# Kernel optimization log

Measured on AMD Instinct MI355X. Metric: run time of the kernel, lower is better.

Reference implementation:

```python
import jax, jax.numpy as jnp
import numpy as np

N_GAUSS = 2048
FEAT_DIM = 3
IMG_H, IMG_W = 256, 256
EPS = 1e-4  # args.eps with tiled rasterizer path


def setup_inputs() -> dict:
    key = jax.random.key(0)
    k_xy, k_sc, k_rot, k_feat = jax.random.split(key, 4)
    xy = jax.random.uniform(k_xy, (N_GAUSS, 2), dtype=jnp.float32)  # normalized [0,1) coords
    # scale holds INVERSE std-devs (disable_inverse_scale=False path: scale = 1/init_scale);
    # values 10..50 give Gaussians spanning a few pixels at 256x256.
    scale = jax.random.uniform(k_sc, (N_GAUSS, 2), minval=10.0, maxval=50.0, dtype=jnp.float32)
    rot = jax.random.normal(k_rot, (N_GAUSS, 1), dtype=jnp.float32)
    feat = jax.random.uniform(k_feat, (N_GAUSS, FEAT_DIM), dtype=jnp.float32)
    return {"xy": xy, "scale": scale, "rot": rot, "feat": feat, "topk": 8}


def reference(xy, scale, rot, feat, topk):
    # Pixel centers in normalized coordinates, matching get_grid(h, w) -> (x, y)
    xs = (jnp.arange(IMG_W, dtype=jnp.float32) + 0.5) / IMG_W
    ys = (jnp.arange(IMG_H, dtype=jnp.float32) + 0.5) / IMG_H
    px, py = jnp.meshgrid(xs, ys, indexing="xy")  # each [H, W]
    px = px.reshape(-1)  # [P]
    py = py.reshape(-1)

    dx = px[:, None] - xy[None, :, 0]  # [P, N]
    dy = py[:, None] - xy[None, :, 1]  # [P, N]

    c = jnp.cos(rot[:, 0])  # [N]
    s = jnp.sin(rot[:, 0])
    # Rotate offset into the Gaussian's local frame
    lx = dx * c + dy * s   # [P, N]
    ly = -dx * s + dy * c  # [P, N]

    # Anisotropic Gaussian weight; scale is the inverse std-dev per axis
    w = jnp.exp(-0.5 * ((lx * scale[:, 0]) ** 2 + (ly * scale[:, 1]) ** 2))  # [P, N]

    # Keep top-k Gaussians per pixel, normalize their weights, accumulate features
    tw, ti = jax.lax.top_k(w, topk)        # [P, K]
    tf = feat[ti]                          # [P, K, C]
    alpha = tw / (jnp.sum(tw, axis=-1, keepdims=True) + EPS)  # [P, K]
    img = jnp.einsum("pk,pkc->pc", alpha, tf)                 # [P, C]
    return img.reshape(IMG_H, IMG_W, FEAT_DIM).transpose(2, 0, 1)  # [C, H, W]
```

## Files before the change

kernel.cpp:

```cpp
#include <hip/hip_runtime.h>
#include <math.h>

#define N_GAUSS 2048
#define IMG_H 256
#define IMG_W 256
#define NPIX (IMG_H * IMG_W)
#define EPS 1e-4f

#define TILE 8
#define TILES_X (IMG_W / TILE)
#define NTILES (TILES_X * (IMG_H / TILE))
#define D_HALF 0.019336f

struct GParam {
    float x, y;
    float c, s;
    float sx, sy;
    float pad0, pad1;
};

__global__ void prep_kernel(const float* __restrict__ xy,
                            const float* __restrict__ scale,
                            const float* __restrict__ rot,
                            GParam* __restrict__ gp) {
    int g = blockIdx.x * blockDim.x + threadIdx.x;
    if (g >= N_GAUSS) return;
    GParam o;
    o.x  = xy[2 * g + 0];
    o.y  = xy[2 * g + 1];
    o.sx = scale[2 * g + 0];
    o.sy = scale[2 * g + 1];
    double r = (double)rot[g];
    o.c = (float)cos(r);
    o.s = (float)sin(r);
    o.pad0 = 0.f; o.pad1 = 0.f;
    gp[g] = o;
}

#define LADDER(T, G)                                                     \
    if ((T) < v7) {                                                      \
        const bool c0 = (T) < v0, c1 = (T) < v1, c2 = (T) < v2;          \
        const bool c3 = (T) < v3, c4 = (T) < v4, c5 = (T) < v5;          \
        const bool c6 = (T) < v6;                                        \
        v7 = c6 ? v6 : (T);            i7 = c6 ? i6 : (G);               \
        v6 = c6 ? (c5 ? v5 : (T)) : v6; i6 = c6 ? (c5 ? i5 : (G)) : i6;  \
        v5 = c5 ? (c4 ? v4 : (T)) : v5; i5 = c5 ? (c4 ? i4 : (G)) : i5;  \
        v4 = c4 ? (c3 ? v3 : (T)) : v4; i4 = c4 ? (c3 ? i3 : (G)) : i4;  \
        v3 = c3 ? (c2 ? v2 : (T)) : v3; i3 = c3 ? (c2 ? i2 : (G)) : i3;  \
        v2 = c2 ? (c1 ? v1 : (T)) : v2; i2 = c2 ? (c1 ? i1 : (G)) : i2;  \
        v1 = c1 ? (c0 ? v0 : (T)) : v1; i1 = c1 ? (c0 ? i0 : (G)) : i1;  \
        v0 = c0 ? (T) : v0;            i0 = c0 ? (G) : i0;               \
    }

#define VLADDER(T)                                                       \
    if ((T) < v7) {                                                      \
        const bool c0 = (T) < v0, c1 = (T) < v1, c2 = (T) < v2;          \
        const bool c3 = (T) < v3, c4 = (T) < v4, c5 = (T) < v5;          \
        const bool c6 = (T) < v6;                                        \
        v7 = c6 ? v6 : (T);                                              \
        v6 = c6 ? (c5 ? v5 : (T)) : v6;                                  \
        v5 = c5 ? (c4 ? v4 : (T)) : v5;                                  \
        v4 = c4 ? (c3 ? v3 : (T)) : v4;                                  \
        v3 = c3 ? (c2 ? v2 : (T)) : v3;                                  \
        v2 = c2 ? (c1 ? v1 : (T)) : v2;                                  \
        v1 = c1 ? (c0 ? v0 : (T)) : v1;                                  \
        v0 = c0 ? (T) : v0;                                              \
    }

__launch_bounds__(256)
__global__ void fused_kernel(const GParam* __restrict__ gp,
                             const float* __restrict__ feat,
                             float* __restrict__ out) {
    __shared__ float rlo[N_GAUSS];
    __shared__ float lists[256][9];
    __shared__ unsigned short qidx[N_GAUSS];
    __shared__ unsigned qcount;
    __shared__ float4 qa[256];
    __shared__ float2 qb[256];
    __shared__ unsigned short qi[256];
    __shared__ float          lt[4][8][64];
    __shared__ unsigned short li[4][8][64];

    const int tid  = threadIdx.x;
    const int lane = tid & 63;
    const int w    = tid >> 6;
    const int tile = blockIdx.x;

    const float cx = (float)((tile & (TILES_X - 1)) * TILE + 4) * (1.0f / IMG_W);
    const float cy = (float)((tile / TILES_X) * TILE + 4) * (1.0f / IMG_H);
    {
        float v0 = INFINITY, v1 = INFINITY, v2 = INFINITY, v3 = INFINITY;
        float v4 = INFINITY, v5 = INFINITY, v6 = INFINITY, v7 = INFINITY;
        for (int r = 0; r < N_GAUSS / 256; ++r) {
            int g = r * 256 + tid;
            GParam q = gp[g];
            float dx = cx - q.x;
            float dy = cy - q.y;
            float lx = dx * q.c + dy * q.s;
            float ly = dy * q.c - dx * q.s;
            float a  = lx * q.sx;
            float b  = ly * q.sy;
            float rr = sqrtf(a * a + b * b);
            float m  = fmaxf(q.sx, q.sy) * D_HALF;
            rlo[g]   = rr - m;
            float rp = rr + m;
            VLADDER(rp)
        }
        lists[tid][0] = v0; lists[tid][1] = v1; lists[tid][2] = v2; lists[tid][3] = v3;
        lists[tid][4] = v4; lists[tid][5] = v5; lists[tid][6] = v6; lists[tid][7] = v7;
        lists[tid][8] = INFINITY;
    }
    __syncthreads();

    for (int stride = 128; stride >= 1; stride >>= 1) {
        if (tid < stride) {
            float outv[8];
            int ia = 0, ib = 0;
#pragma unroll
            for (int k = 0; k < 8; ++k) {
                float av = lists[tid][ia];
                float bv = lists[tid + stride][ib];
                bool ta = av <= bv;
                outv[k] = ta ? av : bv;
                ia += ta ? 1 : 0;
                ib += ta ? 0 : 1;
            }
#pragma unroll
            for (int k = 0; k < 8; ++k) lists[tid][k] = outv[k];
        }
        __syncthreads();
    }
    float cut = lists[0][7];
    cut = cut + 0.01f + 1e-4f * cut;

    if (tid < 64) {
        unsigned base = 0;
        for (int s2 = 0; s2 < N_GAUSS / 64; ++s2) {
            int g = s2 * 64 + tid;
            bool keep = rlo[g] <= cut;
            unsigned long long mask = __ballot(keep);
            unsigned pos = (unsigned)__popcll(mask & ((1ull << tid) - 1ull));
            if (keep) qidx[base + pos] = (unsigned short)g;
            base += (unsigned)__popcll(mask);
        }
        if (tid == 0) qcount = base;
    }
    __syncthreads();

    const int pxi = (tile & (TILES_X - 1)) * TILE + (lane & 7);
    const int pyi = (tile / TILES_X) * TILE + (lane >> 3);
    const int p   = pyi * IMG_W + pxi;
    const float px = (pxi + 0.5f) * (1.0f / IMG_W);
    const float py = (pyi + 0.5f) * (1.0f / IMG_H);

    const int L  = (int)qcount;
    const int L4 = (L + 3) >> 2;
    int start = w * L4; if (start > L) start = L;
    int end   = start + L4; if (end > L) end = L;

    float v0 = INFINITY, v1 = INFINITY, v2 = INFINITY, v3 = INFINITY;
    float v4 = INFINITY, v5 = INFINITY, v6 = INFINITY, v7 = INFINITY;
    int   i0 = 0, i1 = 0, i2 = 0, i3 = 0, i4 = 0, i5 = 0, i6 = 0, i7 = 0;

    for (int base = 0; base < L; base += 256) {
        int t = base + tid;
        if (t < L) {
            int g = qidx[t];
            const float4* g4 = (const float4*)(gp + g);
            float4 a4 = g4[0];
            float4 b4 = g4[1];
            qa[tid] = a4;
            qb[tid] = make_float2(b4.x, b4.y);
            qi[tid] = (unsigned short)g;
        }
        __syncthreads();
        int jlo = start > base ? start : base;
        int lim = base + 256; if (lim > end) lim = end;
        for (int j = jlo; j < lim; ++j) {
            int k = j - base;
            float4 a4 = qa[k];
            float2 b2 = qb[k];
            int g = (int)qi[k];
            float dx = __fsub_rn(px, a4.x);
            float dy = __fsub_rn(py, a4.y);
            float lx = __fadd_rn(__fmul_rn(dx, a4.z), __fmul_rn(dy, a4.w));
            float ly = __fadd_rn(__fmul_rn(-dx, a4.w), __fmul_rn(dy, a4.z));
            float aa = __fmul_rn(lx, b2.x);
            float bb = __fmul_rn(ly, b2.y);
            float t2 = __fadd_rn(__fmul_rn(aa, aa), __fmul_rn(bb, bb));
            LADDER(t2, g)
        }
        __syncthreads();
    }

    lt[w][0][lane] = v0; li[w][0][lane] = (unsigned short)i0;
    lt[w][1][lane] = v1; li[w][1][lane] = (unsigned short)i1;
    lt[w][2][lane] = v2; li[w][2][lane] = (unsigned short)i2;
    lt[w][3][lane] = v3; li[w][3][lane] = (unsigned short)i3;
    lt[w][4][lane] = v4; li[w][4][lane] = (unsigned short)i4;
    lt[w][5][lane] = v5; li[w][5][lane] = (unsigned short)i5;
    lt[w][6][lane] = v6; li[w][6][lane] = (unsigned short)i6;
    lt[w][7][lane] = v7; li[w][7][lane] = (unsigned short)i7;
    __syncthreads();

    if (w == 0) {
        v0 = INFINITY; v1 = INFINITY; v2 = INFINITY; v3 = INFINITY;
        v4 = INFINITY; v5 = INFINITY; v6 = INFINITY; v7 = INFINITY;
        i0 = 0; i1 = 0; i2 = 0; i3 = 0; i4 = 0; i5 = 0; i6 = 0; i7 = 0;
        for (int c = 0; c < 4; ++c) {
#pragma unroll
            for (int k = 0; k < 8; ++k) {
                float t2 = lt[c][k][lane];
                int   g  = (int)li[c][k][lane];
                LADDER(t2, g)
            }
        }
        float w0 = expf(-0.5f * v0), w1 = expf(-0.5f * v1);
        float w2 = expf(-0.5f * v2), w3 = expf(-0.5f * v3);
        float w4 = expf(-0.5f * v4), w5 = expf(-0.5f * v5);
        float w6 = expf(-0.5f * v6), w7 = expf(-0.5f * v7);
        float sum = w0 + w1 + w2 + w3 + w4 + w5 + w6 + w7;
        float inv = 1.0f / (sum + EPS);

        float oc0 = 0.f, oc1 = 0.f, oc2 = 0.f;
#define ACC(K)                                                  \
        {                                                       \
            float al = w##K * inv;                              \
            const float* f = feat + 3 * i##K;                   \
            oc0 = fmaf(al, f[0], oc0);                          \
            oc1 = fmaf(al, f[1], oc1);                          \
            oc2 = fmaf(al, f[2], oc2);                          \
        }
        ACC(0) ACC(1) ACC(2) ACC(3) ACC(4) ACC(5) ACC(6) ACC(7)
#undef ACC

        out[p]            = oc0;
        out[p + NPIX]     = oc1;
        out[p + 2 * NPIX] = oc2;
    }
}

extern "C" void kernel_launch(void* const* d_in, const int* in_sizes, int n_in,
                              void* d_out, int out_size, void* d_ws, size_t ws_size,
                              hipStream_t stream) {
    const float* xy    = (const float*)d_in[0];
    const float* scale = (const float*)d_in[1];
    const float* rot   = (const float*)d_in[2];
    const float* feat  = (const float*)d_in[3];
    float* out = (float*)d_out;
    GParam* gp = (GParam*)d_ws;

    prep_kernel<<<(N_GAUSS + 255) / 256, 256, 0, stream>>>(xy, scale, rot, gp);
    fused_kernel<<<NTILES, 256, 0, stream>>>(gp, feat, out);
}
```

Before: 29.19 us.

## Replace shared-memory tree merge and staging with wave shuffles and per-wave segments

Replaces the 8-step shared-memory tree merge of per-thread top-8 lists with an in-register butterfly bitonic merge using wave shuffles, followed by a single-thread merge of the four per-wave results. Candidate compaction is split so each wave filters its own 512-Gaussian segment in parallel instead of one wave doing all 2048. The main loop then has each wave load its own candidates into registers and broadcast them with shuffles, removing the shared staging buffers and the per-iteration block barriers. The risk is load imbalance between waves when candidates cluster in one segment, plus the extra shuffle instructions per candidate.

```diff
diff --git a/kernel.cpp b/kernel.cpp
--- a/kernel.cpp
+++ b/kernel.cpp
@@ -10,6 +10,7 @@
 #define TILE 8
 #define TILES_X (IMG_W / TILE)
 #define NTILES (TILES_X * (IMG_H / TILE))
+#define SEG 512
 #define D_HALF 0.019336f
 
 struct GParam {
@@ -67,17 +68,32 @@
         v0 = c0 ? (T) : v0;                                              \
     }
 
+#define CE(a, i, j)                                   \
+    { float lo_ = fminf(a[i], a[j]);                  \
+      float hi_ = fmaxf(a[i], a[j]);                  \
+      a[i] = lo_; a[j] = hi_; }
+
+#define MERGE8(A, B)                                  \
+    { float t_[8];                                    \
+      t_[0] = fminf(A[0], B[7]); t_[1] = fminf(A[1], B[6]); \
+      t_[2] = fminf(A[2], B[5]); t_[3] = fminf(A[3], B[4]); \
+      t_[4] = fminf(A[4], B[3]); t_[5] = fminf(A[5], B[2]); \
+      t_[6] = fminf(A[6], B[1]); t_[7] = fminf(A[7], B[0]); \
+      CE(t_,0,4) CE(t_,1,5) CE(t_,2,6) CE(t_,3,7)     \
+      CE(t_,0,2) CE(t_,1,3) CE(t_,4,6) CE(t_,5,7)     \
+      CE(t_,0,1) CE(t_,2,3) CE(t_,4,5) CE(t_,6,7)     \
+      A[0]=t_[0]; A[1]=t_[1]; A[2]=t_[2]; A[3]=t_[3]; \
+      A[4]=t_[4]; A[5]=t_[5]; A[6]=t_[6]; A[7]=t_[7]; }
+
 __launch_bounds__(256)
 __global__ void fused_kernel(const GParam* __restrict__ gp,
                              const float* __restrict__ feat,
                              float* __restrict__ out) {
     __shared__ float rlo[N_GAUSS];
-    __shared__ float lists[256][9];
+    __shared__ float wlist[4][8];
+    __shared__ float s_cut;
     __shared__ unsigned short qidx[N_GAUSS];
-    __shared__ unsigned qcount;
-    __shared__ float4 qa[256];
-    __shared__ float2 qb[256];
-    __shared__ unsigned short qi[256];
+    __shared__ int qcnt[4];
     __shared__ float          lt[4][8][64];
     __shared__ unsigned short li[4][8][64];
 
@@ -88,9 +104,11 @@
 
     const float cx = (float)((tile & (TILES_X - 1)) * TILE + 4) * (1.0f / IMG_W);
     const float cy = (float)((tile / TILES_X) * TILE + 4) * (1.0f / IMG_H);
+    float cur[8];
     {
         float v0 = INFINITY, v1 = INFINITY, v2 = INFINITY, v3 = INFINITY;
         float v4 = INFINITY, v5 = INFINITY, v6 = INFINITY, v7 = INFINITY;
+#pragma unroll
         for (int r = 0; r < N_GAUSS / 256; ++r) {
             int g = r * 256 + tid;
             GParam q = gp[g];
@@ -106,44 +124,60 @@
             float rp = rr + m;
             VLADDER(rp)
         }
-        lists[tid][0] = v0; lists[tid][1] = v1; lists[tid][2] = v2; lists[tid][3] = v3;
-        lists[tid][4] = v4; lists[tid][5] = v5; lists[tid][6] = v6; lists[tid][7] = v7;
-        lists[tid][8] = INFINITY;
-    }
-    __syncthreads();
-
-    for (int stride = 128; stride >= 1; stride >>= 1) {
-        if (tid < stride) {
-            float outv[8];
-            int ia = 0, ib = 0;
-#pragma unroll
-            for (int k = 0; k < 8; ++k) {
-                float av = lists[tid][ia];
-                float bv = lists[tid + stride][ib];
-                bool ta = av <= bv;
-                outv[k] = ta ? av : bv;
-                ia += ta ? 1 : 0;
-                ib += ta ? 0 : 1;
-            }
-#pragma unroll
-            for (int k = 0; k < 8; ++k) lists[tid][k] = outv[k];
-        }
-        __syncthreads();
-    }
-    float cut = lists[0][7];
-    cut = cut + 0.01f + 1e-4f * cut;
-
-    if (tid < 64) {
+        cur[0] = v0; cur[1] = v1; cur[2] = v2; cur[3] = v3;
+        cur[4] = v4; cur[5] = v5; cur[6] = v6; cur[7] = v7;
+    }
+
+#pragma unroll
+    for (int m = 1; m < 64; m <<= 1) {
+        float oth[8];
+#pragma unroll
+        for (int k = 0; k < 8; ++k) oth[k] = __shfl_xor(cur[k], m, 64);
+        float t_[8];
+#pragma unroll
+        for (int k = 0; k < 8; ++k) t_[k] = fminf(cur[k], oth[7 - k]);
+        CE(t_,0,4) CE(t_,1,5) CE(t_,2,6) CE(t_,3,7)
+        CE(t_,0,2) CE(t_,1,3) CE(t_,4,6) CE(t_,5,7)
+        CE(t_,0,1) CE(t_,2,3) CE(t_,4,5) CE(t_,6,7)
+#pragma unroll
+        for (int k = 0; k < 8; ++k) cur[k] = t_[k];
+    }
+    if (lane == 0) {
+#pragma unroll
+        for (int k = 0; k < 8; ++k) wlist[w][k] = cur[k];
+    }
+    __syncthreads();
+
+    if (tid == 0) {
+        float A[8], B[8], C2[8], D2[8];
+#pragma unroll
+        for (int k = 0; k < 8; ++k) {
+            A[k]  = wlist[0][k];
+            B[k]  = wlist[1][k];
+            C2[k] = wlist[2][k];
+            D2[k] = wlist[3][k];
+        }
+        MERGE8(A, B)
+        MERGE8(C2, D2)
+        MERGE8(A, C2)
+        float cut = A[7];
+        s_cut = cut + 0.01f + 1e-4f * cut;
+    }
+    __syncthreads();
+    const float cut = s_cut;
+
+    {
+        const int segbase = w * SEG;
         unsigned base = 0;
-        for (int s2 = 0; s2 < N_GAUSS / 64; ++s2) {
-            int g = s2 * 64 + tid;
+        for (int s2 = 0; s2 < SEG / 64; ++s2) {
+            int g = segbase + s2 * 64 + lane;
             bool keep = rlo[g] <= cut;
             unsigned long long mask = __ballot(keep);
-            unsigned pos = (unsigned)__popcll(mask & ((1ull << tid) - 1ull));
-            if (keep) qidx[base + pos] = (unsigned short)g;
+            unsigned pos = (unsigned)__popcll(mask & ((1ull << lane) - 1ull));
+            if (keep) qidx[segbase + base + pos] = (unsigned short)g;
             base += (unsigned)__popcll(mask);
         }
-        if (tid == 0) qcount = base;
+        if (lane == 0) qcnt[w] = (int)base;
     }
     __syncthreads();
 
@@ -153,44 +187,39 @@
     const float px = (pxi + 0.5f) * (1.0f / IMG_W);
     const float py = (pyi + 0.5f) * (1.0f / IMG_H);
 
-    const int L  = (int)qcount;
-    const int L4 = (L + 3) >> 2;
-    int start = w * L4; if (start > L) start = L;
-    int end   = start + L4; if (end > L) end = L;
-
     float v0 = INFINITY, v1 = INFINITY, v2 = INFINITY, v3 = INFINITY;
     float v4 = INFINITY, v5 = INFINITY, v6 = INFINITY, v7 = INFINITY;
     int   i0 = 0, i1 = 0, i2 = 0, i3 = 0, i4 = 0, i5 = 0, i6 = 0, i7 = 0;
 
-    for (int base = 0; base < L; base += 256) {
-        int t = base + tid;
-        if (t < L) {
-            int g = qidx[t];
-            const float4* g4 = (const float4*)(gp + g);
-            float4 a4 = g4[0];
-            float4 b4 = g4[1];
-            qa[tid] = a4;
-            qb[tid] = make_float2(b4.x, b4.y);
-            qi[tid] = (unsigned short)g;
-        }
-        __syncthreads();
-        int jlo = start > base ? start : base;
-        int lim = base + 256; if (lim > end) lim = end;
-        for (int j = jlo; j < lim; ++j) {
-            int k = j - base;
-            float4 a4 = qa[k];
-            float2 b2 = qb[k];
-            int g = (int)qi[k];
-            float dx = __fsub_rn(px, a4.x);
-            float dy = __fsub_rn(py, a4.y);
-            float lx = __fadd_rn(__fmul_rn(dx, a4.z), __fmul_rn(dy, a4.w));
-            float ly = __fadd_rn(__fmul_rn(-dx, a4.w), __fmul_rn(dy, a4.z));
-            float aa = __fmul_rn(lx, b2.x);
-            float bb = __fmul_rn(ly, b2.y);
-            float t2 = __fadd_rn(__fmul_rn(aa, aa), __fmul_rn(bb, bb));
-            LADDER(t2, g)
-        }
-        __syncthreads();
+    {
+        const int segbase = w * SEG;
+        const int cnt = qcnt[w];
+        for (int b = 0; b < cnt; b += 64) {
+            int t = b + lane;
+            int gg = (t < cnt) ? (int)qidx[segbase + t] : 0;
+            const float4* g4 = (const float4*)(gp + gg);
+            float4 pa  = g4[0];
+            float4 pb4 = g4[1];
+            float pbx = pb4.x, pby = pb4.y;
+            int lim = cnt - b; if (lim > 64) lim = 64;
+            for (int j = 0; j < lim; ++j) {
+                float ax = __shfl(pa.x, j, 64);
+                float ay = __shfl(pa.y, j, 64);
+                float ac = __shfl(pa.z, j, 64);
+                float sn = __shfl(pa.w, j, 64);
+                float bx = __shfl(pbx, j, 64);
+                float by = __shfl(pby, j, 64);
+                int   g  = __shfl(gg,  j, 64);
+                float dx = __fsub_rn(px, ax);
+                float dy = __fsub_rn(py, ay);
+                float lx = __fadd_rn(__fmul_rn(dx, ac), __fmul_rn(dy, sn));
+                float ly = __fadd_rn(__fmul_rn(-dx, sn), __fmul_rn(dy, ac));
+                float aa = __fmul_rn(lx, bx);
+                float bb = __fmul_rn(ly, by);
+                float t2 = __fadd_rn(__fmul_rn(aa, aa), __fmul_rn(bb, bb));
+                LADDER(t2, g)
+            }
+        }
     }
 
     lt[w][0][lane] = v0; li[w][0][lane] = (unsigned short)i0;
@@ -250,6 +279,6 @@
     float* out = (float*)d_out;
     GParam* gp = (GParam*)d_ws;
 
-    prep_kernel<<<(N_GAUSS + 255) / 256, 256, 0, stream>>>(xy, scale, rot, gp);
+    prep_kernel<<<32, 64, 0, stream>>>(xy, scale, rot, gp);
     fused_kernel<<<NTILES, 256, 0, stream>>>(gp, feat, out);
 }
```

New measurement: 28.79 us. About the same (-1.4%).
